# Performance work log

Hardware: AMD Instinct MI355X
Metric: run time of the kernel (lower is better)

Reference implementation:

```python
import jax, jax.numpy as jnp
import numpy as np

N_NODES = 20000
N_EDGES = 320000
IN_DIM = 256
HIDDEN = 256
OUT_DIM = 128
N_LAYERS = 3
N_GROUPS = 4
EXP_PER_GROUP = 2
N_EXPERTS = N_GROUPS * EXP_PER_GROUP
TOP_K = 2


def setup_inputs() -> dict:
    key = jax.random.key(0)
    ks = jax.random.split(key, 12)
    d = HIDDEN
    r = 2 * d  # router/expert input dim: concat(node, neighbor-mean)
    x = jax.random.normal(ks[0], (N_NODES, IN_DIM), dtype=jnp.float32)
    edge_index = jax.random.randint(ks[1], (2, N_EDGES), 0, N_NODES, dtype=jnp.int32)
    s = 0.05
    Wg = jax.random.normal(ks[2], (N_LAYERS, r, N_GROUPS), dtype=jnp.float32) * s
    We = jax.random.normal(ks[3], (N_LAYERS, r, N_EXPERTS), dtype=jnp.float32) * s
    Ww = jax.random.normal(ks[4], (N_LAYERS, r, d), dtype=jnp.float32) * s
    W1 = jax.random.normal(ks[5], (N_LAYERS, N_EXPERTS, r, d), dtype=jnp.float32) * s
    b1 = jnp.zeros((N_LAYERS, N_EXPERTS, d), dtype=jnp.float32)
    W2 = jax.random.normal(ks[6], (N_LAYERS, N_EXPERTS, d, d), dtype=jnp.float32) * s
    b2 = jnp.zeros((N_LAYERS, N_EXPERTS, d), dtype=jnp.float32)
    wc = jax.random.normal(ks[7], (N_LAYERS, r, 1), dtype=jnp.float32) * s
    Wout = jax.random.normal(ks[8], (d, OUT_DIM), dtype=jnp.float32) * s
    return {"x": x, "edge_index": edge_index, "Wg": Wg, "We": We, "Ww": Ww,
            "W1": W1, "b1": b1, "W2": W2, "b2": b2, "wc": wc, "Wout": Wout}


def _moe_layer(h, src, dst, deg, Wg, We, Ww, W1, b1, W2, b2, wc):
    N = h.shape[0]
    # graph message passing: mean aggregation over incoming edges
    agg = jax.ops.segment_sum(h[src], dst, num_segments=N) / deg  # [N, d]
    r = jnp.concatenate([h, agg], axis=-1)  # [N, 2d] combined router input
    # hierarchical routing: group softmax x within-group expert softmax
    gp = jax.nn.softmax(r @ Wg, axis=-1)                                # [N, G]
    ep = jax.nn.softmax((r @ We).reshape(N, N_GROUPS, EXP_PER_GROUP), axis=-1)
    probs = (gp[..., None] * ep).reshape(N, N_EXPERTS)                  # [N, E]
    # top-k gating, renormalized
    topv, topi = jax.lax.top_k(probs, TOP_K)
    gates = jnp.zeros_like(probs).at[jnp.arange(N)[:, None], topi].set(topv)
    gates = gates / (gates.sum(-1, keepdims=True) + 1e-9)              # [N, E]
    # strong experts: per-expert 2-layer MLP, combined by gates
    hid = jax.nn.relu(jnp.einsum('nf,efd->ned', r, W1) + b1[None])      # [N, E, d]
    exp_out = jnp.einsum('ned,edo->neo', hid, W2) + b2[None]            # [N, E, d]
    strong = jnp.einsum('ne,neo->no', gates, exp_out)                   # [N, d]
    # weak shared expert + confidence gate blend
    weak = r @ Ww                                                       # [N, d]
    conf = jax.nn.sigmoid(r @ wc)                                       # [N, 1]
    return jax.nn.relu(conf * strong + (1.0 - conf) * weak)


def reference(x, edge_index, Wg, We, Ww, W1, b1, W2, b2, wc, Wout):
    src, dst = edge_index[0], edge_index[1]
    N = x.shape[0]
    deg = jax.ops.segment_sum(jnp.ones((edge_index.shape[1],), jnp.float32), dst,
                              num_segments=N)
    deg = jnp.maximum(deg, 1.0)[:, None]
    h = x
    for l in range(Wg.shape[0]):  # small fixed layer loop
        h = _moe_layer(h, src, dst, deg, Wg[l], We[l], Ww[l],
                       W1[l], b1[l], W2[l], b2[l], wc[l])
    return h @ Wout
```

## Files before the change

kernel.cpp:

```cpp
#include <hip/hip_runtime.h>

#define NN 20000
#define NEDGE 320000
#define D 256
#define RD 512
#define OD 128
#define NEXP 8
#define NSLOT (2*NN)
#define NODE_BLOCKS 79
#define ASSIGN_BLOCKS 157

typedef unsigned short u16;
typedef __attribute__((ext_vector_type(8))) short short8v;
typedef __attribute__((ext_vector_type(16))) float f32x16;

__device__ __forceinline__ void split1(float v, u16& h, u16& m, u16& l) {
    unsigned b = __float_as_uint(v);
    h = (u16)(b >> 16);
    float fh = __uint_as_float(b & 0xffff0000u);
    float r1 = v - fh;
    unsigned b1 = __float_as_uint(r1);
    m = (u16)(b1 >> 16);
    float fm = __uint_as_float(b1 & 0xffff0000u);
    float r2 = r1 - fm;
    l = (u16)(__float_as_uint(r2) >> 16);
}

__device__ __forceinline__ void split8(const float4& x, const float4& y,
                                       short8v& h, short8v& m, short8v& l) {
    float v[8] = {x.x, x.y, x.z, x.w, y.x, y.y, y.z, y.w};
#pragma unroll
    for (int i = 0; i < 8; i++) {
        u16 hh, mm, ll;
        split1(v[i], hh, mm, ll);
        h[i] = (short)hh; m[i] = (short)mm; l[i] = (short)ll;
    }
}


__global__ void copy_x_zero_cnt_k(const float* __restrict__ x, float* __restrict__ r,
                                  int* __restrict__ cnt) {
    int gid = blockIdx.x * 256 + threadIdx.x;
    int n = gid >> 6;
    int c4 = gid & 63;
    if (gid < NN * (D / 4)) {
        float4 v = reinterpret_cast<const float4*>(x)[gid];
        reinterpret_cast<float4*>(r + (size_t)n * RD)[c4] = v;
    }
    if (gid < NN) cnt[gid] = 0;
}

__global__ void count_edges_k(const int* __restrict__ dst, int* __restrict__ cnt) {
    int e = blockIdx.x * 256 + threadIdx.x;
    if (e < NEDGE) atomicAdd(&cnt[dst[e]], 1);
}

__global__ void block_sums_k(const int* __restrict__ cnt, int* __restrict__ bsum) {
    __shared__ int s[256];
    int i = blockIdx.x * 256 + threadIdx.x;
    s[threadIdx.x] = (i < NN) ? cnt[i] : 0;
    __syncthreads();
    for (int off = 128; off > 0; off >>= 1) {
        if (threadIdx.x < off) s[threadIdx.x] += s[threadIdx.x + off];
        __syncthreads();
    }
    if (threadIdx.x == 0) bsum[blockIdx.x] = s[0];
}

__global__ void scan_bsums_k(int* __restrict__ bsum, int* __restrict__ row_start) {
    if (blockIdx.x == 0 && threadIdx.x == 0) {
        int acc = 0;
        for (int i = 0; i < NODE_BLOCKS; i++) { int t = bsum[i]; bsum[i] = acc; acc += t; }
        row_start[NN] = acc;
    }
}

__global__ void block_scan_k(const int* __restrict__ cnt, const int* __restrict__ bsum,
                             int* __restrict__ row_start, int* __restrict__ cur) {
    __shared__ int s[256];
    int i = blockIdx.x * 256 + threadIdx.x;
    int v = (i < NN) ? cnt[i] : 0;
    s[threadIdx.x] = v;
    __syncthreads();
    for (int off = 1; off < 256; off <<= 1) {
        int t = (threadIdx.x >= off) ? s[threadIdx.x - off] : 0;
        __syncthreads();
        s[threadIdx.x] += t;
        __syncthreads();
    }
    int excl = s[threadIdx.x] - v + bsum[blockIdx.x];
    if (i < NN) { row_start[i] = excl; cur[i] = excl; }
}

__global__ void fill_csr_k(const int* __restrict__ src, const int* __restrict__ dst,
                           int* __restrict__ cur, int* __restrict__ csr_src) {
    int e = blockIdx.x * 256 + threadIdx.x;
    if (e < NEDGE) {
        int pos = atomicAdd(&cur[dst[e]], 1);
        csr_src[pos] = src[e];
    }
}

__global__ void aggregate_k(float* __restrict__ r, const int* __restrict__ row_start,
                            const int* __restrict__ csr_src, int* __restrict__ ec) {
    if (blockIdx.x == 0 && threadIdx.x < 16) ec[threadIdx.x] = 0;
    int wid = blockIdx.x * 4 + (threadIdx.x >> 6);
    int lane = threadIdx.x & 63;
    if (wid >= NN) return;
    int beg = row_start[wid], end = row_start[wid + 1];
    float ax = 0.f, ay = 0.f, az = 0.f, aw = 0.f;
    for (int j = beg; j < end; j++) {
        int s = csr_src[j];
        float4 v = reinterpret_cast<const float4*>(r + (size_t)s * RD)[lane];
        ax += v.x; ay += v.y; az += v.z; aw += v.w;
    }
    float deg = (float)((end - beg) > 1 ? (end - beg) : 1);
    float4 o = make_float4(ax / deg, ay / deg, az / deg, aw / deg);
    reinterpret_cast<float4*>(r + (size_t)wid * RD + D)[lane] = o;
}

__global__ void router_k(const float* __restrict__ r, const float* __restrict__ Wg,
                         const float* __restrict__ We, const float* __restrict__ wc,
                         int* __restrict__ node_top, float* __restrict__ node_gate,
                         float* __restrict__ conf) {
    int wid = blockIdx.x * 4 + (threadIdx.x >> 6);
    int lane = threadIdx.x & 63;
    if (wid >= NN) return;

    const float* rrow = r + (size_t)wid * RD;
    float pg[4] = {0, 0, 0, 0};
    float pe[8] = {0, 0, 0, 0, 0, 0, 0, 0};
    float pc = 0.f;
#pragma unroll
    for (int i = 0; i < 8; i++) {
        int k = lane + i * 64;
        float rv = rrow[k];
        float4 wg = *reinterpret_cast<const float4*>(Wg + (size_t)k * 4);
        pg[0] = fmaf(rv, wg.x, pg[0]); pg[1] = fmaf(rv, wg.y, pg[1]);
        pg[2] = fmaf(rv, wg.z, pg[2]); pg[3] = fmaf(rv, wg.w, pg[3]);
        float4 w0 = *reinterpret_cast<const float4*>(We + (size_t)k * 8);
        float4 w1 = *reinterpret_cast<const float4*>(We + (size_t)k * 8 + 4);
        pe[0] = fmaf(rv, w0.x, pe[0]); pe[1] = fmaf(rv, w0.y, pe[1]);
        pe[2] = fmaf(rv, w0.z, pe[2]); pe[3] = fmaf(rv, w0.w, pe[3]);
        pe[4] = fmaf(rv, w1.x, pe[4]); pe[5] = fmaf(rv, w1.y, pe[5]);
        pe[6] = fmaf(rv, w1.z, pe[6]); pe[7] = fmaf(rv, w1.w, pe[7]);
        pc = fmaf(rv, wc[k], pc);
    }
#pragma unroll
    for (int off = 32; off > 0; off >>= 1) {
#pragma unroll
        for (int g = 0; g < 4; g++) pg[g] += __shfl_xor(pg[g], off);
#pragma unroll
        for (int g = 0; g < 8; g++) pe[g] += __shfl_xor(pe[g], off);
        pc += __shfl_xor(pc, off);
    }

    if (lane == 0) {
        float m = fmaxf(fmaxf(pg[0], pg[1]), fmaxf(pg[2], pg[3]));
        float eg[4]; float sg = 0.f;
#pragma unroll
        for (int g = 0; g < 4; g++) { eg[g] = expf(pg[g] - m); sg += eg[g]; }
        float probs[8];
#pragma unroll
        for (int g = 0; g < 4; g++) {
            float a = pe[2 * g], b = pe[2 * g + 1];
            float mm = fmaxf(a, b);
            float ea = expf(a - mm), eb = expf(b - mm);
            float inv = 1.f / (ea + eb);
            float gp = eg[g] / sg;
            probs[2 * g]     = gp * ea * inv;
            probs[2 * g + 1] = gp * eb * inv;
        }
        int i0 = 0; float v0 = probs[0];
#pragma unroll
        for (int j = 1; j < 8; j++) if (probs[j] > v0) { v0 = probs[j]; i0 = j; }
        int i1 = -1; float v1 = -1e30f;
#pragma unroll
        for (int j = 0; j < 8; j++) if (j != i0 && probs[j] > v1) { v1 = probs[j]; i1 = j; }
        float s = v0 + v1 + 1e-9f;
        node_top[2 * wid] = i0;  node_top[2 * wid + 1] = i1;
        node_gate[2 * wid] = v0 / s;  node_gate[2 * wid + 1] = v1 / s;
        conf[wid] = 1.f / (1.f + expf(-pc));
    }
}

__global__ void expert_hist_k(const int* __restrict__ node_top, int* __restrict__ ec) {
    __shared__ int h[NEXP];
    if (threadIdx.x < NEXP) h[threadIdx.x] = 0;
    __syncthreads();
    int i = blockIdx.x * 256 + threadIdx.x;
    if (i < NSLOT) atomicAdd(&h[node_top[i]], 1);
    __syncthreads();
    if (threadIdx.x < NEXP && h[threadIdx.x] > 0) atomicAdd(&ec[threadIdx.x], h[threadIdx.x]);
}

__global__ void expert_scan_k(const int* __restrict__ ec, int* __restrict__ es,
                              int* __restrict__ ecur) {
    if (blockIdx.x == 0 && threadIdx.x == 0) {
        int acc = 0;
        for (int e = 0; e < NEXP; e++) { es[e] = acc; acc += ec[e]; ecur[e] = 0; }
        es[NEXP] = acc;
    }
}

__global__ void fill_experts_k(const int* __restrict__ node_top, const float* __restrict__ node_gate,
                               const int* __restrict__ es, int* __restrict__ ecur,
                               int* __restrict__ slot_node, float* __restrict__ slot_gate,
                               int* __restrict__ node_slot) {
    __shared__ int hcnt[NEXP], hbase[NEXP];
    int tid = threadIdx.x;
    if (tid < NEXP) hcnt[tid] = 0;
    __syncthreads();
    int i = blockIdx.x * 256 + tid;
    int e = 0, local = 0;
    bool act = (i < NSLOT);
    if (act) {
        e = node_top[i];
        local = atomicAdd(&hcnt[e], 1);
    }
    __syncthreads();
    if (tid < NEXP) hbase[tid] = (hcnt[tid] > 0) ? atomicAdd(&ecur[tid], hcnt[tid]) : 0;
    __syncthreads();
    if (act) {
        int slot = es[e] + hbase[e] + local;
        slot_node[slot] = i >> 1;
        slot_gate[slot] = node_gate[i];
        node_slot[i] = slot;
    }
}

__global__ void combine_k(const float* __restrict__ expout, const float* __restrict__ weak,
                          const float* __restrict__ conf, const int* __restrict__ node_slot,
                          float* __restrict__ r) {
    int gid = blockIdx.x * 256 + threadIdx.x;
    if (gid >= NN * (D / 4)) return;
    int n = gid >> 6, c4 = gid & 63;
    int s0 = node_slot[2 * n], s1 = node_slot[2 * n + 1];
    float4 e0 = reinterpret_cast<const float4*>(expout + (size_t)s0 * D)[c4];
    float4 e1 = reinterpret_cast<const float4*>(expout + (size_t)s1 * D)[c4];
    float4 w  = reinterpret_cast<const float4*>(weak + (size_t)n * D)[c4];
    float cf = conf[n], cg = 1.f - cf;
    float4 o;
    o.x = fmaxf(cf * (e0.x + e1.x) + cg * w.x, 0.f);
    o.y = fmaxf(cf * (e0.y + e1.y) + cg * w.y, 0.f);
    o.z = fmaxf(cf * (e0.z + e1.z) + cg * w.z, 0.f);
    o.w = fmaxf(cf * (e0.w + e1.w) + cg * w.w, 0.f);
    reinterpret_cast<float4*>(r + (size_t)n * RD)[c4] = o;
}

__global__ void btile_k(const float* __restrict__ src, u16* __restrict__ dH,
                        u16* __restrict__ dM, u16* __restrict__ dL,
                        int K, int N, int total) {
    int gid = blockIdx.x * 256 + threadIdx.x;
    if (gid >= total) return;
    int l = gid & 63;
    int tile = gid >> 6;
    int K16 = K >> 4;
    int kb = tile % K16;
    int t2 = tile / K16;
    int N32 = N >> 5;
    int nb = t2 % N32;
    int mat = t2 / N32;
    int kbase = (kb << 4) + ((l >> 5) << 3);
    int n = (nb << 5) + (l & 31);
    const float* s = src + ((size_t)mat * K + kbase) * N + n;
    short8v vh, vm, vl;
#pragma unroll
    for (int j = 0; j < 8; j++) {
        u16 hh, mm, ll;
        split1(s[(size_t)j * N], hh, mm, ll);
        vh[j] = (short)hh; vm[j] = (short)mm; vl[j] = (short)ll;
    }
    size_t o = (size_t)gid * 8;
    *reinterpret_cast<short8v*>(dH + o) = vh;
    *reinterpret_cast<short8v*>(dM + o) = vm;
    *reinterpret_cast<short8v*>(dL + o) = vl;
}

template <int MODE>
__global__ __launch_bounds__(256, 5) void gemm_mfma(
    const float* __restrict__ A, int lda,
    const u16* __restrict__ BH, const u16* __restrict__ BM,
    const u16* __restrict__ BL,
    const float* __restrict__ bias,
    float* __restrict__ C, int ldc,
    const int* __restrict__ es,
    const int* __restrict__ slot_node,
    const float* __restrict__ slot_gate,
    int M, int N, int K) {
    int tid = threadIdx.x;
    int row0, valid_rows;
    if (MODE == 0) {
        row0 = blockIdx.x * 64;
        valid_rows = M - row0; if (valid_rows > 64) valid_rows = 64;
    } else {
        int bx = blockIdx.x, acc0 = 0, expert = -1, mt = 0;
        row0 = 0; valid_rows = 0;
        for (int e = 0; e < NEXP; e++) {
            int c = es[e + 1] - es[e];
            int t = (c + 63) >> 6;
            if (bx < acc0 + t) {
                expert = e; mt = bx - acc0; row0 = es[e] + (mt << 6);
                valid_rows = c - (mt << 6); if (valid_rows > 64) valid_rows = 64;
                break;
            }
            acc0 += t;
        }
        if (expert < 0) return;
        int bo = expert * N * K;
        BH += bo; BM += bo; BL += bo;
        bias += expert * D;
    }
    int ncol0 = blockIdx.y * 128;

    int lane = tid & 63;
    int wave = tid >> 6;
    int wr = (wave & 1) * 32;
    int wc = (wave >> 1) * 64;
    int fl = lane & 31;
    int kh8 = (lane >> 5) * 8;

    int arow;
    {
        int i0 = row0 + wr + fl;
        if (MODE == 1) {
            i0 = i0 < NSLOT ? i0 : NSLOT - 1;
            arow = slot_node[i0];
        } else {
            arow = i0 < M ? i0 : M - 1;
        }
    }
    const float* pA = A + (size_t)arow * lda + kh8;

    int K16 = K >> 4;
    int nb0 = (ncol0 + wc) >> 5;
    int tbase0 = nb0 * K16 * 512 + lane * 8;
    int tbase1 = (nb0 + 1) * K16 * 512 + lane * 8;

    f32x16 acc0 = {};
    f32x16 acc1 = {};

#pragma unroll 2
    for (int kt = 0; kt < K; kt += 16) {
        float4 a0 = *reinterpret_cast<const float4*>(pA + kt);
        float4 a1 = *reinterpret_cast<const float4*>(pA + kt + 4);
        int ko = (kt >> 4) * 512;
        short8v bH0 = *reinterpret_cast<const short8v*>(BH + tbase0 + ko);
        short8v bM0 = *reinterpret_cast<const short8v*>(BM + tbase0 + ko);
        short8v bL0 = *reinterpret_cast<const short8v*>(BL + tbase0 + ko);
        short8v bH1 = *reinterpret_cast<const short8v*>(BH + tbase1 + ko);
        short8v bM1 = *reinterpret_cast<const short8v*>(BM + tbase1 + ko);
        short8v bL1 = *reinterpret_cast<const short8v*>(BL + tbase1 + ko);
        short8v aH, aM, aL;
        split8(a0, a1, aH, aM, aL);
#define MFMA_ACC(d, a, b) d = __builtin_amdgcn_mfma_f32_32x32x16_bf16(a, b, d, 0, 0, 0)
        MFMA_ACC(acc0, aH, bH0); MFMA_ACC(acc0, aH, bM0);
        MFMA_ACC(acc0, aM, bH0); MFMA_ACC(acc0, aH, bL0);
        MFMA_ACC(acc0, aM, bM0); MFMA_ACC(acc0, aL, bH0);
        MFMA_ACC(acc1, aH, bH1); MFMA_ACC(acc1, aH, bM1);
        MFMA_ACC(acc1, aM, bH1); MFMA_ACC(acc1, aH, bL1);
        MFMA_ACC(acc1, aM, bM1); MFMA_ACC(acc1, aL, bH1);
#undef MFMA_ACC
    }

    int fh = lane >> 5;
#pragma unroll
    for (int j = 0; j < 2; j++) {
        const f32x16& a = j ? acc1 : acc0;
        int colg = ncol0 + wc + j * 32 + fl;
        float bv = (MODE != 0) ? bias[colg] : 0.f;
#pragma unroll
        for (int rg = 0; rg < 16; rg++) {
            int lrow = wr + (rg & 3) + 8 * (rg >> 2) + 4 * fh;
            if (lrow >= valid_rows) continue;
            int growo = row0 + lrow;
            float v = a[rg] + bv;
            if (MODE == 1) {
                v = fmaxf(v, 0.f);
            } else if (MODE == 2) {
                v *= slot_gate[growo];
            }
            C[(size_t)growo * ldc + colg] = v;
        }
    }
}

extern "C" void kernel_launch(void* const* d_in, const int* in_sizes, int n_in,
                              void* d_out, int out_size, void* d_ws, size_t ws_size,
                              hipStream_t stream) {
    (void)in_sizes; (void)n_in; (void)out_size; (void)ws_size;
    const float* x    = (const float*)d_in[0];
    const int*   ei   = (const int*)d_in[1];
    const float* Wg   = (const float*)d_in[2];
    const float* We   = (const float*)d_in[3];
    const float* Ww   = (const float*)d_in[4];
    const float* W1   = (const float*)d_in[5];
    const float* b1   = (const float*)d_in[6];
    const float* W2   = (const float*)d_in[7];
    const float* b2   = (const float*)d_in[8];
    const float* wcp  = (const float*)d_in[9];
    const float* Wout = (const float*)d_in[10];
    float* out = (float*)d_out;

    char* p = (char*)d_ws;
    auto alloc = [&](size_t bytes) -> char* {
        char* q = p; p += (bytes + 255) & ~(size_t)255; return q;
    };
    int*   cnt       = (int*)alloc((size_t)NN * 4);
    int*   row_start = (int*)alloc((size_t)(NN + 1) * 4);
    int*   cur       = (int*)alloc((size_t)NN * 4);
    int*   bsum      = (int*)alloc(128 * 4);
    int*   csr_src   = (int*)alloc((size_t)NEDGE * 4);
    float* r         = (float*)alloc((size_t)NN * RD * 4);
    float* hid       = (float*)alloc((size_t)NSLOT * D * 4);
    float* expout    = (float*)alloc((size_t)NSLOT * D * 4);
    float* conf      = (float*)alloc((size_t)NN * 4);
    int*   node_top  = (int*)alloc((size_t)2 * NN * 4);
    float* node_gate = (float*)alloc((size_t)2 * NN * 4);
    int*   node_slot = (int*)alloc((size_t)2 * NN * 4);
    int*   slot_node = (int*)alloc((size_t)NSLOT * 4);
    float* slot_gate = (float*)alloc((size_t)NSLOT * 4);
    int*   ec        = (int*)alloc(64 * 4);
    int*   es        = (int*)alloc(64 * 4);
    int*   ecur      = (int*)alloc(64 * 4);
    u16* w1tH = (u16*)alloc((size_t)NEXP * D * RD * 2);
    u16* w1tM = (u16*)alloc((size_t)NEXP * D * RD * 2);
    u16* w1tL = (u16*)alloc((size_t)NEXP * D * RD * 2);
    u16* w2tH = (u16*)alloc((size_t)NEXP * D * D * 2);
    u16* w2tM = (u16*)alloc((size_t)NEXP * D * D * 2);
    u16* w2tL = (u16*)alloc((size_t)NEXP * D * D * 2);
    u16* wwtH = (u16*)alloc((size_t)D * RD * 2);
    u16* wwtM = (u16*)alloc((size_t)D * RD * 2);
    u16* wwtL = (u16*)alloc((size_t)D * RD * 2);
    u16* wotH = (u16*)alloc((size_t)OD * D * 2);
    u16* wotM = (u16*)alloc((size_t)OD * D * 2);
    u16* wotL = (u16*)alloc((size_t)OD * D * 2);
    float* weak = hid;

    const int* srcp = ei;
    const int* dstp = ei + NEDGE;
    const int EB = (NEDGE + 255) / 256;

    copy_x_zero_cnt_k<<<5000, 256, 0, stream>>>(x, r, cnt);
    count_edges_k<<<EB, 256, 0, stream>>>(dstp, cnt);
    block_sums_k<<<NODE_BLOCKS, 256, 0, stream>>>(cnt, bsum);
    scan_bsums_k<<<1, 64, 0, stream>>>(bsum, row_start);
    block_scan_k<<<NODE_BLOCKS, 256, 0, stream>>>(cnt, bsum, row_start, cur);
    fill_csr_k<<<EB, 256, 0, stream>>>(srcp, dstp, cur, csr_src);
    btile_k<<<16, 256, 0, stream>>>(Wout, wotH, wotM, wotL, D, OD, 4096);

    for (int l = 0; l < 3; l++) {
        btile_k<<<512, 256, 0, stream>>>(W1 + (size_t)l * NEXP * RD * D,
                                         w1tH, w1tM, w1tL, RD, D, 131072);
        btile_k<<<256, 256, 0, stream>>>(W2 + (size_t)l * NEXP * D * D,
                                         w2tH, w2tM, w2tL, D, D, 65536);
        btile_k<<<64, 256, 0, stream>>>(Ww + (size_t)l * RD * D,
                                        wwtH, wwtM, wwtL, RD, D, 16384);
        aggregate_k<<<5000, 256, 0, stream>>>(r, row_start, csr_src, ec);
        router_k<<<5000, 256, 0, stream>>>(r,
            Wg + (size_t)l * RD * 4, We + (size_t)l * RD * 8, wcp + (size_t)l * RD,
            node_top, node_gate, conf);
        expert_hist_k<<<ASSIGN_BLOCKS, 256, 0, stream>>>(node_top, ec);
        expert_scan_k<<<1, 64, 0, stream>>>(ec, es, ecur);
        fill_experts_k<<<ASSIGN_BLOCKS, 256, 0, stream>>>(node_top, node_gate, es, ecur,
                                                          slot_node, slot_gate, node_slot);
        gemm_mfma<1><<<dim3(640, 2), 256, 0, stream>>>(r, RD, w1tH, w1tM, w1tL,
            b1 + (size_t)l * NEXP * D, hid, D, es, slot_node, slot_gate, NSLOT, D, RD);
        gemm_mfma<2><<<dim3(640, 2), 256, 0, stream>>>(hid, D, w2tH, w2tM, w2tL,
            b2 + (size_t)l * NEXP * D, expout, D, es, slot_node, slot_gate, NSLOT, D, D);
        gemm_mfma<0><<<dim3(313, 2), 256, 0, stream>>>(r, RD, wwtH, wwtM, wwtL,
            nullptr, weak, D, nullptr, nullptr, nullptr, NN, D, RD);
        combine_k<<<5000, 256, 0, stream>>>(expout, weak, conf, node_slot, r);
    }
    gemm_mfma<0><<<dim3(313, 1), 256, 0, stream>>>(r, RD, wotH, wotM, wotL,
        nullptr, out, OD, nullptr, nullptr, nullptr, NN, OD, D);
}
```

Measured before the change: 915.0 us.

## Stage split A tile in LDS and widen GEMM block to 128 rows

Each GEMM block now covers 128 rows instead of 64, and each wave computes a 64x64 output with four accumulators. The A tile is loaded once per block, split into bf16 hi/mid/lo parts and written to shared memory, so each B fragment is reused across twice as many rows. This halves B traffic per row and cuts redundant splitting work. In exchange it adds two __syncthreads per k-step with no double buffering, lowers the occupancy target to 3 blocks, and wastes more work on padded tail tiles for each expert.

```diff
diff --git a/kernel.cpp b/kernel.cpp
--- a/kernel.cpp
+++ b/kernel.cpp
@@ -278,7 +278,7 @@
 }
 
 template <int MODE>
-__global__ __launch_bounds__(256, 5) void gemm_mfma(
+__global__ __launch_bounds__(256, 3) void gemm_mfma(
     const float* __restrict__ A, int lda,
     const u16* __restrict__ BH, const u16* __restrict__ BM,
     const u16* __restrict__ BL,
@@ -288,20 +288,23 @@
     const int* __restrict__ slot_node,
     const float* __restrict__ slot_gate,
     int M, int N, int K) {
+    constexpr int PL2 = 2048;
+    __shared__ u16 sA[3 * PL2];
+
     int tid = threadIdx.x;
     int row0, valid_rows;
     if (MODE == 0) {
-        row0 = blockIdx.x * 64;
-        valid_rows = M - row0; if (valid_rows > 64) valid_rows = 64;
+        row0 = blockIdx.x * 128;
+        valid_rows = M - row0; if (valid_rows > 128) valid_rows = 128;
     } else {
         int bx = blockIdx.x, acc0 = 0, expert = -1, mt = 0;
         row0 = 0; valid_rows = 0;
         for (int e = 0; e < NEXP; e++) {
             int c = es[e + 1] - es[e];
-            int t = (c + 63) >> 6;
+            int t = (c + 127) >> 7;
             if (bx < acc0 + t) {
-                expert = e; mt = bx - acc0; row0 = es[e] + (mt << 6);
-                valid_rows = c - (mt << 6); if (valid_rows > 64) valid_rows = 64;
+                expert = e; mt = bx - acc0; row0 = es[e] + (mt << 7);
+                valid_rows = c - (mt << 7); if (valid_rows > 128) valid_rows = 128;
                 break;
             }
             acc0 += t;
@@ -313,34 +316,35 @@
     }
     int ncol0 = blockIdx.y * 128;
 
+    int srow = tid >> 1;
+    int koff = (tid & 1) * 8;
+    int grow;
+    {
+        int i0 = row0 + srow;
+        if (MODE == 1) {
+            i0 = i0 < NSLOT ? i0 : NSLOT - 1;
+            grow = slot_node[i0];
+        } else {
+            grow = i0 < M ? i0 : M - 1;
+        }
+    }
+    const float* pA = A + (size_t)grow * lda + koff;
+    int woff = ((srow >> 5) * 2 + (koff >> 3)) * 256 + (srow & 31) * 8;
+
     int lane = tid & 63;
     int wave = tid >> 6;
-    int wr = (wave & 1) * 32;
+    int wr = (wave & 1) * 64;
     int wc = (wave >> 1) * 64;
     int fl = lane & 31;
-    int kh8 = (lane >> 5) * 8;
-
-    int arow;
-    {
-        int i0 = row0 + wr + fl;
-        if (MODE == 1) {
-            i0 = i0 < NSLOT ? i0 : NSLOT - 1;
-            arow = slot_node[i0];
-        } else {
-            arow = i0 < M ? i0 : M - 1;
-        }
-    }
-    const float* pA = A + (size_t)arow * lda + kh8;
-
     int K16 = K >> 4;
     int nb0 = (ncol0 + wc) >> 5;
     int tbase0 = nb0 * K16 * 512 + lane * 8;
     int tbase1 = (nb0 + 1) * K16 * 512 + lane * 8;
-
-    f32x16 acc0 = {};
-    f32x16 acc1 = {};
-
-#pragma unroll 2
+    int roff0 = ((wr >> 5) * 2 + (lane >> 5)) * 256 + fl * 8;
+    int roff1 = (((wr + 32) >> 5) * 2 + (lane >> 5)) * 256 + fl * 8;
+
+    f32x16 acc00 = {}, acc01 = {}, acc10 = {}, acc11 = {};
+
     for (int kt = 0; kt < K; kt += 16) {
         float4 a0 = *reinterpret_cast<const float4*>(pA + kt);
         float4 a1 = *reinterpret_cast<const float4*>(pA + kt + 4);
@@ -351,36 +355,58 @@
         short8v bH1 = *reinterpret_cast<const short8v*>(BH + tbase1 + ko);
         short8v bM1 = *reinterpret_cast<const short8v*>(BM + tbase1 + ko);
         short8v bL1 = *reinterpret_cast<const short8v*>(BL + tbase1 + ko);
-        short8v aH, aM, aL;
-        split8(a0, a1, aH, aM, aL);
+        __syncthreads();
+        {
+            short8v h, m, l;
+            split8(a0, a1, h, m, l);
+            *reinterpret_cast<short8v*>(&sA[0 * PL2 + woff]) = h;
+            *reinterpret_cast<short8v*>(&sA[1 * PL2 + woff]) = m;
+            *reinterpret_cast<short8v*>(&sA[2 * PL2 + woff]) = l;
+        }
+        __syncthreads();
+        short8v aH0 = *reinterpret_cast<const short8v*>(&sA[0 * PL2 + roff0]);
+        short8v aM0 = *reinterpret_cast<const short8v*>(&sA[1 * PL2 + roff0]);
+        short8v aL0 = *reinterpret_cast<const short8v*>(&sA[2 * PL2 + roff0]);
+        short8v aH1 = *reinterpret_cast<const short8v*>(&sA[0 * PL2 + roff1]);
+        short8v aM1 = *reinterpret_cast<const short8v*>(&sA[1 * PL2 + roff1]);
+        short8v aL1 = *reinterpret_cast<const short8v*>(&sA[2 * PL2 + roff1]);
 #define MFMA_ACC(d, a, b) d = __builtin_amdgcn_mfma_f32_32x32x16_bf16(a, b, d, 0, 0, 0)
-        MFMA_ACC(acc0, aH, bH0); MFMA_ACC(acc0, aH, bM0);
-        MFMA_ACC(acc0, aM, bH0); MFMA_ACC(acc0, aH, bL0);
-        MFMA_ACC(acc0, aM, bM0); MFMA_ACC(acc0, aL, bH0);
-        MFMA_ACC(acc1, aH, bH1); MFMA_ACC(acc1, aH, bM1);
-        MFMA_ACC(acc1, aM, bH1); MFMA_ACC(acc1, aH, bL1);
-        MFMA_ACC(acc1, aM, bM1); MFMA_ACC(acc1, aL, bH1);
+        MFMA_ACC(acc00, aH0, bH0); MFMA_ACC(acc00, aH0, bM0);
+        MFMA_ACC(acc00, aM0, bH0); MFMA_ACC(acc00, aH0, bL0);
+        MFMA_ACC(acc00, aM0, bM0); MFMA_ACC(acc00, aL0, bH0);
+        MFMA_ACC(acc01, aH0, bH1); MFMA_ACC(acc01, aH0, bM1);
+        MFMA_ACC(acc01, aM0, bH1); MFMA_ACC(acc01, aH0, bL1);
+        MFMA_ACC(acc01, aM0, bM1); MFMA_ACC(acc01, aL0, bH1);
+        MFMA_ACC(acc10, aH1, bH0); MFMA_ACC(acc10, aH1, bM0);
+        MFMA_ACC(acc10, aM1, bH0); MFMA_ACC(acc10, aH1, bL0);
+        MFMA_ACC(acc10, aM1, bM0); MFMA_ACC(acc10, aL1, bH0);
+        MFMA_ACC(acc11, aH1, bH1); MFMA_ACC(acc11, aH1, bM1);
+        MFMA_ACC(acc11, aM1, bH1); MFMA_ACC(acc11, aH1, bL1);
+        MFMA_ACC(acc11, aM1, bM1); MFMA_ACC(acc11, aL1, bH1);
 #undef MFMA_ACC
     }
 
     int fh = lane >> 5;
 #pragma unroll
-    for (int j = 0; j < 2; j++) {
-        const f32x16& a = j ? acc1 : acc0;
-        int colg = ncol0 + wc + j * 32 + fl;
-        float bv = (MODE != 0) ? bias[colg] : 0.f;
-#pragma unroll
-        for (int rg = 0; rg < 16; rg++) {
-            int lrow = wr + (rg & 3) + 8 * (rg >> 2) + 4 * fh;
-            if (lrow >= valid_rows) continue;
-            int growo = row0 + lrow;
-            float v = a[rg] + bv;
-            if (MODE == 1) {
-                v = fmaxf(v, 0.f);
-            } else if (MODE == 2) {
-                v *= slot_gate[growo];
+    for (int i = 0; i < 2; i++) {
+#pragma unroll
+        for (int j = 0; j < 2; j++) {
+            const f32x16& a = i ? (j ? acc11 : acc10) : (j ? acc01 : acc00);
+            int colg = ncol0 + wc + j * 32 + fl;
+            float bv = (MODE != 0) ? bias[colg] : 0.f;
+#pragma unroll
+            for (int rg = 0; rg < 16; rg++) {
+                int lrow = wr + i * 32 + (rg & 3) + 8 * (rg >> 2) + 4 * fh;
+                if (lrow >= valid_rows) continue;
+                int growo = row0 + lrow;
+                float v = a[rg] + bv;
+                if (MODE == 1) {
+                    v = fmaxf(v, 0.f);
+                } else if (MODE == 2) {
+                    v *= slot_gate[growo];
+                }
+                C[(size_t)growo * ldc + colg] = v;
             }
-            C[(size_t)growo * ldc + colg] = v;
         }
     }
 }
@@ -464,14 +490,14 @@
         expert_scan_k<<<1, 64, 0, stream>>>(ec, es, ecur);
         fill_experts_k<<<ASSIGN_BLOCKS, 256, 0, stream>>>(node_top, node_gate, es, ecur,
                                                           slot_node, slot_gate, node_slot);
-        gemm_mfma<1><<<dim3(640, 2), 256, 0, stream>>>(r, RD, w1tH, w1tM, w1tL,
+        gemm_mfma<1><<<dim3(320, 2), 256, 0, stream>>>(r, RD, w1tH, w1tM, w1tL,
             b1 + (size_t)l * NEXP * D, hid, D, es, slot_node, slot_gate, NSLOT, D, RD);
-        gemm_mfma<2><<<dim3(640, 2), 256, 0, stream>>>(hid, D, w2tH, w2tM, w2tL,
+        gemm_mfma<2><<<dim3(320, 2), 256, 0, stream>>>(hid, D, w2tH, w2tM, w2tL,
             b2 + (size_t)l * NEXP * D, expout, D, es, slot_node, slot_gate, NSLOT, D, D);
-        gemm_mfma<0><<<dim3(313, 2), 256, 0, stream>>>(r, RD, wwtH, wwtM, wwtL,
+        gemm_mfma<0><<<dim3(157, 2), 256, 0, stream>>>(r, RD, wwtH, wwtM, wwtL,
             nullptr, weak, D, nullptr, nullptr, nullptr, NN, D, RD);
         combine_k<<<5000, 256, 0, stream>>>(expout, weak, conf, node_slot, r);
     }
-    gemm_mfma<0><<<dim3(313, 1), 256, 0, stream>>>(r, RD, wotH, wotM, wotL,
+    gemm_mfma<0><<<dim3(157, 1), 256, 0, stream>>>(r, RD, wotH, wotM, wotL,
         nullptr, out, OD, nullptr, nullptr, nullptr, NN, OD, D);
 }
```

Measured after the change: 890.9 us. 2.6% less time.
